# Kernel tuning notes

Measured on AMD Instinct MI355X. Metric: run time of the kernel, lower is better.

## Reference

```python
import jax, jax.numpy as jnp
import numpy as np

D_MODEL = 1024
H = 16
D_K = D_MODEL // H


def setup_inputs() -> dict:
    key = jax.random.key(0)
    ks = jax.random.split(key, 12)
    B, S = 4, 2048
    s = 1.0 / np.sqrt(D_MODEL)
    return {
        "Q": jax.random.normal(ks[0], (B, S, D_MODEL), jnp.float32),
        "K": jax.random.normal(ks[1], (B, S, D_MODEL), jnp.float32),
        "V": jax.random.normal(ks[2], (B, S, D_MODEL), jnp.float32),
        "attn_mask": jnp.ones((B, S), jnp.int32),
        "Wq": jax.random.normal(ks[3], (D_MODEL, D_MODEL), jnp.float32) * s,
        "bq": jax.random.normal(ks[4], (D_MODEL,), jnp.float32) * s,
        "Wk": jax.random.normal(ks[5], (D_MODEL, D_MODEL), jnp.float32) * s,
        "bk": jax.random.normal(ks[6], (D_MODEL,), jnp.float32) * s,
        "Wv": jax.random.normal(ks[7], (D_MODEL, D_MODEL), jnp.float32) * s,
        "bv": jax.random.normal(ks[8], (D_MODEL,), jnp.float32) * s,
        "Wo": jax.random.normal(ks[9], (D_MODEL, D_MODEL), jnp.float32) * s,
        "bo": jax.random.normal(ks[10], (D_MODEL,), jnp.float32) * s,
    }


def _split_heads(x):
    B, S, _ = x.shape
    return x.reshape(B, S, H, D_K).transpose(0, 2, 1, 3)  # (B,H,S,Dk)


def reference(Q, K, V, attn_mask, Wq, bq, Wk, bk, Wv, bv, Wo, bo):
    # Linear projections (torch Linear: x @ W.T + b)
    q = _split_heads(Q @ Wq.T + bq)
    k = _split_heads(K @ Wk.T + bk)
    v = _split_heads(V @ Wv.T + bv)
    scale = 1.0 / jnp.sqrt(jnp.asarray(D_K, q.dtype))
    scores = jnp.einsum("bhqd,bhkd->bhqk", q, k) * scale  # (B,H,S,S)
    # 2-D mask (B,S) broadcast over heads and query positions; 0 -> -inf
    mask = attn_mask[:, None, None, :]
    scores = jnp.where(mask == 0, -jnp.inf, scores)
    attn = jax.nn.softmax(scores, axis=-1)
    # dropout_proba = 0.0 -> identity
    x = jnp.einsum("bhqk,bhkd->bhqd", attn, v)
    B, _, S, _ = x.shape
    x = x.transpose(0, 2, 1, 3).reshape(B, S, D_MODEL)
    return x @ Wo.T + bo
```

## Files before the change

### kernel.cpp

```cpp
#include <hip/hip_runtime.h>
#include <stdint.h>

typedef unsigned short u16;
typedef __attribute__((ext_vector_type(8))) unsigned short u16x8;
typedef __attribute__((ext_vector_type(4))) unsigned short u16x4;
typedef __attribute__((ext_vector_type(2))) __fp16 h16x2;
typedef __attribute__((ext_vector_type(4))) _Float16 f16x4;
typedef __attribute__((ext_vector_type(8))) _Float16 f16x8;
typedef __attribute__((ext_vector_type(4))) float f32x4;

#define MFMA16F16(a,b,c)  __builtin_amdgcn_mfma_f32_16x16x16f16((a),(b),(c),0,0,0)
#define MFMA32F16(a,b,c)  __builtin_amdgcn_mfma_f32_16x16x32_f16((a),(b),(c),0,0,0)

__device__ __forceinline__ f32x4 f4zero() {
    f32x4 z; z[0]=0.f; z[1]=0.f; z[2]=0.f; z[3]=0.f; return z;
}
__device__ __forceinline__ u16x8 cvth8(float4 a, float4 b) {
    union { h16x2 h[4]; u16x8 u; } U;
    U.h[0] = __builtin_amdgcn_cvt_pkrtz(a.x, a.y);
    U.h[1] = __builtin_amdgcn_cvt_pkrtz(a.z, a.w);
    U.h[2] = __builtin_amdgcn_cvt_pkrtz(b.x, b.y);
    U.h[3] = __builtin_amdgcn_cvt_pkrtz(b.z, b.w);
    return U.u;
}

#define GLDS(gp, lp) __builtin_amdgcn_global_load_lds( \
    (const __attribute__((address_space(1))) void*)(gp), \
    (__attribute__((address_space(3))) void*)(lp), 16, 0, 0)

#define QSC 0.1803368801111601f

__global__ __launch_bounds__(256) void conv_all(
    const float* __restrict__ w0, const float* __restrict__ w1,
    const float* __restrict__ w2, const float* __restrict__ w3,
    const float* __restrict__ x0, const float* __restrict__ x1,
    const float* __restrict__ x2,
    u16* __restrict__ wout, u16* __restrict__ xout)
{
    int bx = blockIdx.x;
    const float* src; u16* dst;
    if (bx < 1024) {
        const int t = bx >> 8;
        src = (t == 0) ? w0 : (t == 1) ? w1 : (t == 2) ? w2 : w3;
        const size_t idx = (size_t)(bx & 255) * 4096 + (size_t)threadIdx.x * 16;
        src += idx;
        dst = wout + (size_t)t * 1048576 + idx;
    } else {
        bx -= 1024;
        const int t = bx >> 11;
        src = (t == 0) ? x0 : (t == 1) ? x1 : x2;
        const size_t idx = (size_t)(bx & 2047) * 4096 + (size_t)threadIdx.x * 16;
        src += idx;
        dst = xout + (size_t)t * 8388608 + idx;
    }
    float4 a0 = *(const float4*)(src);
    float4 a1 = *(const float4*)(src + 4);
    float4 a2 = *(const float4*)(src + 8);
    float4 a3 = *(const float4*)(src + 12);
    *(u16x8*)dst       = cvth8(a0, a1);
    *(u16x8*)(dst + 8) = cvth8(a2, a3);
}

__global__ __launch_bounds__(256) void conv_w(
    const float* __restrict__ w0, const float* __restrict__ w1,
    const float* __restrict__ w2, const float* __restrict__ w3,
    u16* __restrict__ out)
{
    const int t = blockIdx.x >> 8;
    const float* src = (t == 0) ? w0 : (t == 1) ? w1 : (t == 2) ? w2 : w3;
    const size_t idx = (size_t)(blockIdx.x & 255) * 4096 + (size_t)threadIdx.x * 16;
    u16* dst = out + (size_t)t * 1048576 + idx;
    float4 a0 = *(const float4*)(src + idx);
    float4 a1 = *(const float4*)(src + idx + 4);
    float4 a2 = *(const float4*)(src + idx + 8);
    float4 a3 = *(const float4*)(src + idx + 12);
    *(u16x8*)dst       = cvth8(a0, a1);
    *(u16x8*)(dst + 8) = cvth8(a2, a3);
}

template<int MODE>
__global__ __launch_bounds__(256, 3) void gemm_qkv(
    const float* __restrict__ Qf, const float* __restrict__ Kf, const float* __restrict__ Vf,
    const u16* __restrict__ xc, const u16* __restrict__ wc,
    const float* __restrict__ Wqf, const float* __restrict__ Wkf, const float* __restrict__ Wvf,
    const float* __restrict__ bq, const float* __restrict__ bk, const float* __restrict__ bv,
    u16* __restrict__ qhp, u16* __restrict__ khp, u16* __restrict__ vtp)
{
    __shared__ __align__(16) u16 smem[24576];
    u16* Ct = smem;

    const int t  = blockIdx.y >> 3;
    const int n0 = (blockIdx.y & 7) * 128;
    const int m0 = blockIdx.x * 128;
    const float* X    = (t == 0) ? Qf : (t == 1) ? Kf : Vf;
    const float* Wf   = (t == 0) ? Wqf : (t == 1) ? Wkf : Wvf;
    const float* bias = (t == 0) ? bq : (t == 1) ? bk : bv;
    const u16*   Wb   = wc + (size_t)t * 1048576;
    const u16*   Xc   = xc + (size_t)t * 8388608;
    u16*         dst  = (t == 0) ? qhp : (t == 1) ? khp : vtp;
    const float  scl  = (t == 0) ? QSC : 1.0f;

    const int tid  = threadIdx.x;
    const int wave = tid >> 6, lane = tid & 63;
    const int quad = lane >> 4, l16 = lane & 15;
    const int wm = (wave >> 1) * 64, wn = (wave & 1) * 64;

    const int srow = lane >> 2;
    const size_t scol = (size_t)(lane & 3) * 8;
    const int sr = tid >> 1, hh = tid & 1;

    f32x4 acc[4][4];
    for (int i = 0; i < 4; i++) for (int j = 0; j < 4; j++) acc[i][j] = f4zero();

    auto stageA = [&](int b, int kt) {
        GLDS(Xc + (size_t)(m0 + wave * 32 +      srow) * 1024 + kt * 32 + scol,
             smem + b * 8192 + wave * 1024);
        GLDS(Xc + (size_t)(m0 + wave * 32 + 16 + srow) * 1024 + kt * 32 + scol,
             smem + b * 8192 + wave * 1024 + 512);
    };
    auto stageB = [&](int b, int kt) {
        GLDS(Wb + (size_t)(n0 + wave * 32 +      srow) * 1024 + kt * 32 + scol,
             smem + b * 8192 + 4096 + wave * 1024);
        GLDS(Wb + (size_t)(n0 + wave * 32 + 16 + srow) * 1024 + kt * 32 + scol,
             smem + b * 8192 + 4096 + wave * 1024 + 512);
    };
    float4 xr_[4];
    auto loadX = [&](int kt) {
        const float* p = X + (size_t)(m0 + sr) * 1024 + kt * 32 + hh * 16;
        xr_[0] = *(const float4*)(p);     xr_[1] = *(const float4*)(p + 4);
        xr_[2] = *(const float4*)(p + 8); xr_[3] = *(const float4*)(p + 12);
    };
    auto writeX = [&](int b) {
        u16* d = smem + b * 8192 + sr * 32 + hh * 16;
        *(u16x8*)d       = cvth8(xr_[0], xr_[1]);
        *(u16x8*)(d + 8) = cvth8(xr_[2], xr_[3]);
    };
    auto comp = [&](int b) {
        const u16* As = smem + b * 8192;
        const u16* Bs = As + 4096;
        f16x8 af[4], bfr[4];
#pragma unroll
        for (int i = 0; i < 4; i++) {
            af[i]  = *(const f16x8*)(As + (wm + i * 16 + l16) * 32 + quad * 8);
            bfr[i] = *(const f16x8*)(Bs + (wn + i * 16 + l16) * 32 + quad * 8);
        }
        __builtin_amdgcn_s_setprio(1);
#pragma unroll
        for (int i = 0; i < 4; i++)
#pragma unroll
            for (int j = 0; j < 4; j++)
                acc[i][j] = MFMA32F16(af[i], bfr[j], acc[i][j]);
        __builtin_amdgcn_s_setprio(0);
    };

    if (MODE == 0) {
        for (int kt = 0; kt < 32; ++kt) {
            loadX(kt); writeX(0);
            const float* p = Wf + (size_t)(n0 + sr) * 1024 + kt * 32 + hh * 16;
            float4 b0 = *(const float4*)(p);     float4 b1 = *(const float4*)(p + 4);
            float4 b2 = *(const float4*)(p + 8); float4 b3 = *(const float4*)(p + 12);
            u16* d = smem + 4096 + sr * 32 + hh * 16;
            *(u16x8*)d       = cvth8(b0, b1);
            *(u16x8*)(d + 8) = cvth8(b2, b3);
            __syncthreads();
            comp(0);
            __syncthreads();
        }
    } else {
        if (MODE == 2) stageA(0, 0);
        stageB(0, 0);
        if (MODE == 2) stageA(1, 1);
        stageB(1, 1);
        if (MODE == 1) { loadX(0); writeX(0); }
        int bA = 0, bB = 1, bC = 2;
        for (int kt = 0; kt < 31; ++kt) {
            if (MODE == 2) asm volatile("s_waitcnt vmcnt(4) lgkmcnt(0)" ::: "memory");
            else           asm volatile("s_waitcnt vmcnt(2) lgkmcnt(0)" ::: "memory");
            __builtin_amdgcn_s_barrier();
            __builtin_amdgcn_sched_barrier(0);
            if (MODE == 1) loadX(kt + 1);
            if (kt < 30) {
                if (MODE == 2) stageA(bC, kt + 2);
                stageB(bC, kt + 2);
            }
            comp(bA);
            if (MODE == 1) writeX(bB);
            int tmp = bA; bA = bB; bB = bC; bC = tmp;
        }
        asm volatile("s_waitcnt vmcnt(0) lgkmcnt(0)" ::: "memory");
        __builtin_amdgcn_s_barrier();
        __builtin_amdgcn_sched_barrier(0);
        comp(bA);
    }
    __syncthreads();

#pragma unroll
    for (int i = 0; i < 4; i++) {
        const int row = wm + i * 16 + quad * 4;
#pragma unroll
        for (int j = 0; j < 4; j++) {
            const int col = wn + j * 16 + l16;
            const float bv2 = bias[n0 + col];
#pragma unroll
            for (int r = 0; r < 2; r++) {
                union { h16x2 h; unsigned u; } P;
                P.h = __builtin_amdgcn_cvt_pkrtz((acc[i][j][2*r] + bv2) * scl,
                                                 (acc[i][j][2*r+1] + bv2) * scl);
                Ct[(row + 2*r)     * 136 + col] = (u16)(P.u & 0xFFFF);
                Ct[(row + 2*r + 1) * 136 + col] = (u16)(P.u >> 16);
            }
        }
    }
    __syncthreads();

    if (t < 2) {
        const int row = tid >> 1, half = tid & 1;
        const int m = m0 + row, b = m >> 11, s = m & 2047;
        const int h = (n0 >> 6) + half;
        u16* o = dst + ((size_t)(b * 16 + h) * 2048 + s) * 64;
        const u16* src = Ct + row * 136 + half * 64;
#pragma unroll
        for (int j = 0; j < 64; j += 8) *(u16x8*)(o + j) = *(const u16x8*)(src + j);
    } else {
        const int col = tid >> 1, shalf = tid & 1;
        const int h = (n0 >> 6) + (col >> 6), d = col & 63;
        const int mb = m0 + shalf * 64, b = mb >> 11, sb = mb & 2047;
        u16* o = dst + (size_t)((b * 16 + h) * 64 + d) * 2048 + sb;
#pragma unroll
        for (int j0 = 0; j0 < 64; j0 += 8) {
            u16x8 tv;
#pragma unroll
            for (int j = 0; j < 8; j++) tv[j] = Ct[(shalf * 64 + j0 + j) * 136 + col];
            *(u16x8*)(o + j0) = tv;
        }
    }
}

template<int MODE>
__global__ __launch_bounds__(256, 3) void gemm_o(
    const u16* __restrict__ Xb, const u16* __restrict__ wcO,
    const float* __restrict__ Wf, const float* __restrict__ bias,
    float* __restrict__ out)
{
    __shared__ __align__(16) u16 smem[24576];

    const int tid  = threadIdx.x;
    const int wave = tid >> 6, lane = tid & 63;
    const int quad = lane >> 4, l16 = lane & 15;
    const int m0 = blockIdx.x * 128, n0 = blockIdx.y * 128;
    const int wm = (wave >> 1) * 64, wn = (wave & 1) * 64;

    const int srow = lane >> 2;
    const size_t scol = (size_t)(lane & 3) * 8;
    const int sr = tid >> 1, hh = tid & 1;

    f32x4 acc[4][4];
    for (int i = 0; i < 4; i++) for (int j = 0; j < 4; j++) acc[i][j] = f4zero();

    auto stageA = [&](int b, int kt) {
        GLDS(Xb + (size_t)(m0 + wave * 32 +      srow) * 1024 + kt * 32 + scol,
             smem + b * 8192 + wave * 1024);
        GLDS(Xb + (size_t)(m0 + wave * 32 + 16 + srow) * 1024 + kt * 32 + scol,
             smem + b * 8192 + wave * 1024 + 512);
    };
    auto stageB = [&](int b, int kt) {
        GLDS(wcO + (size_t)(n0 + wave * 32 +      srow) * 1024 + kt * 32 + scol,
             smem + b * 8192 + 4096 + wave * 1024);
        GLDS(wcO + (size_t)(n0 + wave * 32 + 16 + srow) * 1024 + kt * 32 + scol,
             smem + b * 8192 + 4096 + wave * 1024 + 512);
    };
    float4 wr_[4];
    auto loadW = [&](int kt) {
        const float* p = Wf + (size_t)(n0 + sr) * 1024 + kt * 32 + hh * 16;
        wr_[0] = *(const float4*)(p);     wr_[1] = *(const float4*)(p + 4);
        wr_[2] = *(const float4*)(p + 8); wr_[3] = *(const float4*)(p + 12);
    };
    auto writeW = [&](int b) {
        u16* d = smem + b * 8192 + 4096 + sr * 32 + hh * 16;
        *(u16x8*)d       = cvth8(wr_[0], wr_[1]);
        *(u16x8*)(d + 8) = cvth8(wr_[2], wr_[3]);
    };
    auto comp = [&](int b) {
        const u16* As = smem + b * 8192;
        const u16* Bs = As + 4096;
        f16x8 af[4], bfr[4];
#pragma unroll
        for (int i = 0; i < 4; i++) {
            af[i]  = *(const f16x8*)(As + (wm + i * 16 + l16) * 32 + quad * 8);
            bfr[i] = *(const f16x8*)(Bs + (wn + i * 16 + l16) * 32 + quad * 8);
        }
        __builtin_amdgcn_s_setprio(1);
#pragma unroll
        for (int i = 0; i < 4; i++)
#pragma unroll
            for (int j = 0; j < 4; j++)
                acc[i][j] = MFMA32F16(af[i], bfr[j], acc[i][j]);
        __builtin_amdgcn_s_setprio(0);
    };

    stageA(0, 0);
    if (MODE == 2) stageB(0, 0);
    stageA(1, 1);
    if (MODE == 2) stageB(1, 1);
    if (MODE == 1) { loadW(0); writeW(0); }
    int bA = 0, bB = 1, bC = 2;
    for (int kt = 0; kt < 31; ++kt) {
        if (MODE == 2) asm volatile("s_waitcnt vmcnt(4) lgkmcnt(0)" ::: "memory");
        else           asm volatile("s_waitcnt vmcnt(2) lgkmcnt(0)" ::: "memory");
        __builtin_amdgcn_s_barrier();
        __builtin_amdgcn_sched_barrier(0);
        if (MODE == 1) loadW(kt + 1);
        if (kt < 30) {
            stageA(bC, kt + 2);
            if (MODE == 2) stageB(bC, kt + 2);
        }
        comp(bA);
        if (MODE == 1) writeW(bB);
        int tmp = bA; bA = bB; bB = bC; bC = tmp;
    }
    asm volatile("s_waitcnt vmcnt(0) lgkmcnt(0)" ::: "memory");
    __builtin_amdgcn_s_barrier();
    __builtin_amdgcn_sched_barrier(0);
    comp(bA);

#pragma unroll
    for (int i = 0; i < 4; i++)
#pragma unroll
        for (int j = 0; j < 4; j++) {
            const int col = wn + j * 16 + l16;
            const float bv = bias[n0 + col];
#pragma unroll
            for (int r = 0; r < 4; r++)
                out[(size_t)(m0 + wm + i * 16 + quad * 4 + r) * 1024 + n0 + col] = acc[i][j][r] + bv;
        }
}

__global__ __launch_bounds__(256, 4) void attn_fused(
    const u16* __restrict__ qh, const u16* __restrict__ kh,
    const u16* __restrict__ vth, const int* __restrict__ mask,
    u16* __restrict__ xout)
{
    __shared__ __align__(16) u16 Ksh[2][4096];
    __shared__ __align__(16) u16 Vsh[2][4352];
    __shared__ float mshf[2][64];

    const int tid = threadIdx.x, wave = tid >> 6, lane = tid & 63;
    const int quad = lane >> 4, l16 = lane & 15;

    const int flat = blockIdx.x + (blockIdx.y << 4);
    const int xr = flat & 7, xc_ = flat >> 3;
    const int qb = xc_ & 15, bh = xr + ((xc_ >> 4) << 3);
    const int b = bh >> 4, h = bh & 15;
    const int wq = qb * 128 + wave * 32;

    f16x8 qf[2][2];
#pragma unroll
    for (int qg = 0; qg < 2; qg++)
#pragma unroll
        for (int kc = 0; kc < 2; kc++)
            qf[qg][kc] = *(const f16x8*)(qh + ((size_t)bh * 2048 + wq + qg * 16 + l16) * 64
                                         + kc * 32 + quad * 8);

    f32x4 o[2][4];
#pragma unroll
    for (int qg = 0; qg < 2; qg++)
        for (int dt = 0; dt < 4; dt++) o[qg][dt] = f4zero();
    f32x4 lacc[2]; lacc[0] = f4zero(); lacc[1] = f4zero();
    f16x4 ones;
    ones[0] = (_Float16)1.f; ones[1] = (_Float16)1.f;
    ones[2] = (_Float16)1.f; ones[3] = (_Float16)1.f;

    const int klr = lane >> 3;
    const size_t kgoff = (size_t)((lane & 7) ^ klr) << 3;
    const u16* kgb = kh + (size_t)bh * 2048 * 64;

    const int skey = tid >> 2, sc = (tid & 3) * 16;
    const u16* vg = vth + ((size_t)bh * 64 + skey) * 2048 + sc;
    const int mrow = b * 2048;

    {
        GLDS(kgb + (size_t)(wave * 16 + klr) * 64 + kgoff,     &Ksh[0][wave * 1024]);
        GLDS(kgb + (size_t)(wave * 16 + 8 + klr) * 64 + kgoff, &Ksh[0][wave * 1024 + 512]);
        const u16x8 v0 = *(const u16x8*)(vg);
        const u16x8 v1 = *(const u16x8*)(vg + 8);
        u16* vd = &Vsh[0][skey * 68 + sc];
        *(u16x4*)(vd)      = (u16x4){v0[0], v0[1], v0[2], v0[3]};
        *(u16x4*)(vd + 4)  = (u16x4){v0[4], v0[5], v0[6], v0[7]};
        *(u16x4*)(vd + 8)  = (u16x4){v1[0], v1[1], v1[2], v1[3]};
        *(u16x4*)(vd + 12) = (u16x4){v1[4], v1[5], v1[6], v1[7]};
        if (tid < 64) mshf[0][tid] = mask[mrow + tid] ? -10.0f : -1.0e30f;
    }
    __syncthreads();

    for (int t = 0; t < 32; ++t) {
        const int cur = t & 1;
        const u16* Kc = &Ksh[cur][0];
        const u16* Vc = &Vsh[cur][0];

        u16x8 v0, v1; int mreg = 1;
        const int kk2 = (t + 1) * 64;
        if (t < 31) {
            GLDS(kgb + (size_t)(kk2 + wave * 16 + klr) * 64 + kgoff,
                 &Ksh[cur ^ 1][wave * 1024]);
            GLDS(kgb + (size_t)(kk2 + wave * 16 + 8 + klr) * 64 + kgoff,
                 &Ksh[cur ^ 1][wave * 1024 + 512]);
            v0 = *(const u16x8*)(vg + kk2);
            v1 = *(const u16x8*)(vg + kk2 + 8);
            if (tid < 64) mreg = mask[mrow + kk2 + tid];
        }

        __builtin_amdgcn_s_setprio(1);
#pragma unroll
        for (int nt = 0; nt < 4; nt++) {
            const int kro = (nt * 16 + l16) * 64;
            const f16x8 kf0 = *(const f16x8*)(Kc + kro + ((quad ^ (l16 & 7)) << 3));
            const f16x8 kf1 = *(const f16x8*)(Kc + kro + (((quad ^ 4) ^ (l16 & 7)) << 3));
            const float4 mb = *(const float4*)(&mshf[cur][nt * 16 + quad * 4]);
            f16x4 pf[2];
#pragma unroll
            for (int qg = 0; qg < 2; qg++) {
                f32x4 z;
                z[0] = mb.x; z[1] = mb.y; z[2] = mb.z; z[3] = mb.w;
                z = MFMA32F16(kf0, qf[qg][0], z);
                z = MFMA32F16(kf1, qf[qg][1], z);
                union { h16x2 h[2]; f16x4 v; } U;
                U.h[0] = __builtin_amdgcn_cvt_pkrtz(__builtin_amdgcn_exp2f(z[0]),
                                                    __builtin_amdgcn_exp2f(z[1]));
                U.h[1] = __builtin_amdgcn_cvt_pkrtz(__builtin_amdgcn_exp2f(z[2]),
                                                    __builtin_amdgcn_exp2f(z[3]));
                pf[qg] = U.v;
            }
            lacc[0] = MFMA16F16(ones, pf[0], lacc[0]);
            lacc[1] = MFMA16F16(ones, pf[1], lacc[1]);
#pragma unroll
            for (int dt = 0; dt < 4; dt++) {
                const f16x4 vf = *(const f16x4*)(Vc + (dt * 16 + l16) * 68 + nt * 16 + quad * 4);
                o[0][dt] = MFMA16F16(vf, pf[0], o[0][dt]);
                o[1][dt] = MFMA16F16(vf, pf[1], o[1][dt]);
            }
        }
        __builtin_amdgcn_s_setprio(0);

        if (t < 31) {
            u16* vd = &Vsh[cur ^ 1][skey * 68 + sc];
            *(u16x4*)(vd)      = (u16x4){v0[0], v0[1], v0[2], v0[3]};
            *(u16x4*)(vd + 4)  = (u16x4){v0[4], v0[5], v0[6], v0[7]};
            *(u16x4*)(vd + 8)  = (u16x4){v1[0], v1[1], v1[2], v1[3]};
            *(u16x4*)(vd + 12) = (u16x4){v1[4], v1[5], v1[6], v1[7]};
            if (tid < 64) mshf[cur ^ 1][tid] = mreg ? -10.0f : -1.0e30f;
        }
        __syncthreads();
    }

#pragma unroll
    for (int qg = 0; qg < 2; qg++) {
        const float inv = 1.0f / lacc[qg][0];
        const int row = wq + qg * 16 + l16;
        u16* op = xout + ((size_t)b * 2048 + row) * 1024 + h * 64;
#pragma unroll
        for (int dt = 0; dt < 4; dt++) {
            union { h16x2 h[2]; u16x4 u; } U;
            U.h[0] = __builtin_amdgcn_cvt_pkrtz(o[qg][dt][0] * inv, o[qg][dt][1] * inv);
            U.h[1] = __builtin_amdgcn_cvt_pkrtz(o[qg][dt][2] * inv, o[qg][dt][3] * inv);
            *(u16x4*)(op + dt * 16 + quad * 4) = U.u;
        }
    }
}

extern "C" void kernel_launch(void* const* d_in, const int* in_sizes, int n_in,
                              void* d_out, int out_size, void* d_ws, size_t ws_size,
                              hipStream_t stream)
{
    const float* Q   = (const float*)d_in[0];
    const float* K   = (const float*)d_in[1];
    const float* V   = (const float*)d_in[2];
    const int*   msk = (const int*)d_in[3];
    const float* Wq  = (const float*)d_in[4];
    const float* bq  = (const float*)d_in[5];
    const float* Wk  = (const float*)d_in[6];
    const float* bk  = (const float*)d_in[7];
    const float* Wv  = (const float*)d_in[8];
    const float* bv  = (const float*)d_in[9];
    const float* Wo  = (const float*)d_in[10];
    const float* bo  = (const float*)d_in[11];

    u16* base = (u16*)d_ws;
    dim3 blk(256);
    dim3 gq(64, 24);
    dim3 ga(16, 64);
    dim3 go(64, 8);

    if (ws_size >= 109051904UL) {
        u16* wc  = base;
        u16* xc  = base + 4194304;
        u16* qhp = xc + 25165824;
        u16* khp = qhp + 8388608;
        u16* vtp = khp + 8388608;
        u16* xs  = xc;
        conv_all<<<7168, blk, 0, stream>>>(Wq, Wk, Wv, Wo, Q, K, V, wc, xc);
        gemm_qkv<2><<<gq, blk, 0, stream>>>(Q, K, V, xc, wc,
            nullptr, nullptr, nullptr, bq, bk, bv, qhp, khp, vtp);
        attn_fused<<<ga, blk, 0, stream>>>(qhp, khp, vtp, msk, xs);
        gemm_o<2><<<go, blk, 0, stream>>>(xs, wc + 3 * 1048576, nullptr, bo, (float*)d_out);
    } else if (ws_size >= ((size_t)72 << 20)) {
        u16* wc  = base;
        u16* qhp = base + 4194304;
        u16* khp = qhp + 8388608;
        u16* vtp = khp + 8388608;
        u16* xs  = vtp + 8388608;
        conv_w<<<1024, blk, 0, stream>>>(Wq, Wk, Wv, Wo, wc);
        gemm_qkv<1><<<gq, blk, 0, stream>>>(Q, K, V, nullptr, wc,
            nullptr, nullptr, nullptr, bq, bk, bv, qhp, khp, vtp);
        attn_fused<<<ga, blk, 0, stream>>>(qhp, khp, vtp, msk, xs);
        gemm_o<2><<<go, blk, 0, stream>>>(xs, wc + 3 * 1048576, nullptr, bo, (float*)d_out);
    } else {
        u16* qhp = base;
        u16* khp = qhp + 8388608;
        u16* vtp = khp + 8388608;
        u16* xs  = vtp + 8388608;
        gemm_qkv<0><<<gq, blk, 0, stream>>>(Q, K, V, nullptr, nullptr,
            Wq, Wk, Wv, bq, bk, bv, qhp, khp, vtp);
        attn_fused<<<ga, blk, 0, stream>>>(qhp, khp, vtp, msk, xs);
        gemm_o<1><<<go, blk, 0, stream>>>(xs, nullptr, Wo, bo, (float*)d_out);
    }
}
```

Measured before the change: 347.7 us.

## Drop separate activation conversion pass and batch softmax before PV MFMAs

Removes the conv_all path that converted Q/K/V activations to fp16 in a separate kernel, so the QKV GEMM always converts fp32 activations in registers while staging (MODE 1). This avoids an extra full read and write of the activations plus one launch, at the cost of more VALU and load work inside the GEMM. The attention inner loop is also restructured: all four key tiles' exp and probabilities are computed first, then the row-sum and PV MFMAs are issued in batches, which gives the scheduler longer MFMA chains but raises register pressure.

New measurement: 362.0 us. +4.1%, slower.

```diff
diff --git a/kernel.cpp b/kernel.cpp
--- a/kernel.cpp
+++ b/kernel.cpp
@@ -29,37 +29,6 @@
     (__attribute__((address_space(3))) void*)(lp), 16, 0, 0)
 
 #define QSC 0.1803368801111601f
-
-__global__ __launch_bounds__(256) void conv_all(
-    const float* __restrict__ w0, const float* __restrict__ w1,
-    const float* __restrict__ w2, const float* __restrict__ w3,
-    const float* __restrict__ x0, const float* __restrict__ x1,
-    const float* __restrict__ x2,
-    u16* __restrict__ wout, u16* __restrict__ xout)
-{
-    int bx = blockIdx.x;
-    const float* src; u16* dst;
-    if (bx < 1024) {
-        const int t = bx >> 8;
-        src = (t == 0) ? w0 : (t == 1) ? w1 : (t == 2) ? w2 : w3;
-        const size_t idx = (size_t)(bx & 255) * 4096 + (size_t)threadIdx.x * 16;
-        src += idx;
-        dst = wout + (size_t)t * 1048576 + idx;
-    } else {
-        bx -= 1024;
-        const int t = bx >> 11;
-        src = (t == 0) ? x0 : (t == 1) ? x1 : x2;
-        const size_t idx = (size_t)(bx & 2047) * 4096 + (size_t)threadIdx.x * 16;
-        src += idx;
-        dst = xout + (size_t)t * 8388608 + idx;
-    }
-    float4 a0 = *(const float4*)(src);
-    float4 a1 = *(const float4*)(src + 4);
-    float4 a2 = *(const float4*)(src + 8);
-    float4 a3 = *(const float4*)(src + 12);
-    *(u16x8*)dst       = cvth8(a0, a1);
-    *(u16x8*)(dst + 8) = cvth8(a2, a3);
-}
 
 __global__ __launch_bounds__(256) void conv_w(
     const float* __restrict__ w0, const float* __restrict__ w1,
@@ -81,7 +50,7 @@
 template<int MODE>
 __global__ __launch_bounds__(256, 3) void gemm_qkv(
     const float* __restrict__ Qf, const float* __restrict__ Kf, const float* __restrict__ Vf,
-    const u16* __restrict__ xc, const u16* __restrict__ wc,
+    const u16* __restrict__ wc,
     const float* __restrict__ Wqf, const float* __restrict__ Wkf, const float* __restrict__ Wvf,
     const float* __restrict__ bq, const float* __restrict__ bk, const float* __restrict__ bv,
     u16* __restrict__ qhp, u16* __restrict__ khp, u16* __restrict__ vtp)
@@ -96,7 +65,6 @@
     const float* Wf   = (t == 0) ? Wqf : (t == 1) ? Wkf : Wvf;
     const float* bias = (t == 0) ? bq : (t == 1) ? bk : bv;
     const u16*   Wb   = wc + (size_t)t * 1048576;
-    const u16*   Xc   = xc + (size_t)t * 8388608;
     u16*         dst  = (t == 0) ? qhp : (t == 1) ? khp : vtp;
     const float  scl  = (t == 0) ? QSC : 1.0f;
 
@@ -112,12 +80,6 @@
     f32x4 acc[4][4];
     for (int i = 0; i < 4; i++) for (int j = 0; j < 4; j++) acc[i][j] = f4zero();
 
-    auto stageA = [&](int b, int kt) {
-        GLDS(Xc + (size_t)(m0 + wave * 32 +      srow) * 1024 + kt * 32 + scol,
-             smem + b * 8192 + wave * 1024);
-        GLDS(Xc + (size_t)(m0 + wave * 32 + 16 + srow) * 1024 + kt * 32 + scol,
-             smem + b * 8192 + wave * 1024 + 512);
-    };
     auto stageB = [&](int b, int kt) {
         GLDS(Wb + (size_t)(n0 + wave * 32 +      srow) * 1024 + kt * 32 + scol,
              smem + b * 8192 + 4096 + wave * 1024);
@@ -167,24 +129,18 @@
             __syncthreads();
         }
     } else {
-        if (MODE == 2) stageA(0, 0);
         stageB(0, 0);
-        if (MODE == 2) stageA(1, 1);
         stageB(1, 1);
-        if (MODE == 1) { loadX(0); writeX(0); }
+        loadX(0); writeX(0);
         int bA = 0, bB = 1, bC = 2;
         for (int kt = 0; kt < 31; ++kt) {
-            if (MODE == 2) asm volatile("s_waitcnt vmcnt(4) lgkmcnt(0)" ::: "memory");
-            else           asm volatile("s_waitcnt vmcnt(2) lgkmcnt(0)" ::: "memory");
+            asm volatile("s_waitcnt vmcnt(2) lgkmcnt(0)" ::: "memory");
             __builtin_amdgcn_s_barrier();
             __builtin_amdgcn_sched_barrier(0);
-            if (MODE == 1) loadX(kt + 1);
-            if (kt < 30) {
-                if (MODE == 2) stageA(bC, kt + 2);
-                stageB(bC, kt + 2);
-            }
+            loadX(kt + 1);
+            if (kt < 30) stageB(bC, kt + 2);
             comp(bA);
-            if (MODE == 1) writeX(bB);
+            writeX(bB);
             int tmp = bA; bA = bB; bB = bC; bC = tmp;
         }
         asm volatile("s_waitcnt vmcnt(0) lgkmcnt(0)" ::: "memory");
@@ -410,13 +366,13 @@
         }
 
         __builtin_amdgcn_s_setprio(1);
+        f16x4 pf[4][2];
 #pragma unroll
         for (int nt = 0; nt < 4; nt++) {
             const int kro = (nt * 16 + l16) * 64;
             const f16x8 kf0 = *(const f16x8*)(Kc + kro + ((quad ^ (l16 & 7)) << 3));
             const f16x8 kf1 = *(const f16x8*)(Kc + kro + (((quad ^ 4) ^ (l16 & 7)) << 3));
             const float4 mb = *(const float4*)(&mshf[cur][nt * 16 + quad * 4]);
-            f16x4 pf[2];
 #pragma unroll
             for (int qg = 0; qg < 2; qg++) {
                 f32x4 z;
@@ -428,15 +384,21 @@
                                                     __builtin_amdgcn_exp2f(z[1]));
                 U.h[1] = __builtin_amdgcn_cvt_pkrtz(__builtin_amdgcn_exp2f(z[2]),
                                                     __builtin_amdgcn_exp2f(z[3]));
-                pf[qg] = U.v;
+                pf[nt][qg] = U.v;
             }
-            lacc[0] = MFMA16F16(ones, pf[0], lacc[0]);
-            lacc[1] = MFMA16F16(ones, pf[1], lacc[1]);
-#pragma unroll
-            for (int dt = 0; dt < 4; dt++) {
+        }
+#pragma unroll
+        for (int nt = 0; nt < 4; nt++) {
+            lacc[0] = MFMA16F16(ones, pf[nt][0], lacc[0]);
+            lacc[1] = MFMA16F16(ones, pf[nt][1], lacc[1]);
+        }
+#pragma unroll
+        for (int dt = 0; dt < 4; dt++) {
+#pragma unroll
+            for (int nt = 0; nt < 4; nt++) {
                 const f16x4 vf = *(const f16x4*)(Vc + (dt * 16 + l16) * 68 + nt * 16 + quad * 4);
-                o[0][dt] = MFMA16F16(vf, pf[0], o[0][dt]);
-                o[1][dt] = MFMA16F16(vf, pf[1], o[1][dt]);
+                o[0][dt] = MFMA16F16(vf, pf[nt][0], o[0][dt]);
+                o[1][dt] = MFMA16F16(vf, pf[nt][1], o[1][dt]);
             }
         }
         __builtin_amdgcn_s_setprio(0);
@@ -490,26 +452,14 @@
     dim3 ga(16, 64);
     dim3 go(64, 8);
 
-    if (ws_size >= 109051904UL) {
-        u16* wc  = base;
-        u16* xc  = base + 4194304;
-        u16* qhp = xc + 25165824;
-        u16* khp = qhp + 8388608;
-        u16* vtp = khp + 8388608;
-        u16* xs  = xc;
-        conv_all<<<7168, blk, 0, stream>>>(Wq, Wk, Wv, Wo, Q, K, V, wc, xc);
-        gemm_qkv<2><<<gq, blk, 0, stream>>>(Q, K, V, xc, wc,
-            nullptr, nullptr, nullptr, bq, bk, bv, qhp, khp, vtp);
-        attn_fused<<<ga, blk, 0, stream>>>(qhp, khp, vtp, msk, xs);
-        gemm_o<2><<<go, blk, 0, stream>>>(xs, wc + 3 * 1048576, nullptr, bo, (float*)d_out);
-    } else if (ws_size >= ((size_t)72 << 20)) {
+    if (ws_size >= ((size_t)72 << 20)) {
         u16* wc  = base;
         u16* qhp = base + 4194304;
         u16* khp = qhp + 8388608;
         u16* vtp = khp + 8388608;
         u16* xs  = vtp + 8388608;
         conv_w<<<1024, blk, 0, stream>>>(Wq, Wk, Wv, Wo, wc);
-        gemm_qkv<1><<<gq, blk, 0, stream>>>(Q, K, V, nullptr, wc,
+        gemm_qkv<1><<<gq, blk, 0, stream>>>(Q, K, V, wc,
             nullptr, nullptr, nullptr, bq, bk, bv, qhp, khp, vtp);
         attn_fused<<<ga, blk, 0, stream>>>(qhp, khp, vtp, msk, xs);
         gemm_o<2><<<go, blk, 0, stream>>>(xs, wc + 3 * 1048576, nullptr, bo, (float*)d_out);
@@ -518,7 +468,7 @@
         u16* khp = qhp + 8388608;
         u16* vtp = khp + 8388608;
         u16* xs  = vtp + 8388608;
-        gemm_qkv<0><<<gq, blk, 0, stream>>>(Q, K, V, nullptr, nullptr,
+        gemm_qkv<0><<<gq, blk, 0, stream>>>(Q, K, V, nullptr,
             Wq, Wk, Wv, bq, bk, bv, qhp, khp, vtp);
         attn_fused<<<ga, blk, 0, stream>>>(qhp, khp, vtp, msk, xs);
         gemm_o<1><<<go, blk, 0, stream>>>(xs, nullptr, Wo, bo, (float*)d_out);
```
